# Performance work log

Hardware: AMD Instinct MI355X
Metric: run time of the kernel (lower is better)

Reference implementation:

```python
import jax, jax.numpy as jnp
import numpy as np

B, T, C, H = 4, 2048, 768, 12
HD = C // H  # 64
EPS = 1e-5


def layer_norm(x, g, b):
    mu = jnp.mean(x, axis=-1, keepdims=True)
    var = jnp.var(x, axis=-1, keepdims=True)
    return (x - mu) * jax.lax.rsqrt(var + EPS) * g + b


def setup_inputs() -> dict:
    key = jax.random.key(0)
    ks = jax.random.split(key, 14)
    s_c = 1.0 / np.sqrt(C)
    s_4c = 1.0 / np.sqrt(4 * C)
    return {
        "x": jax.random.normal(ks[0], (B, T, C), jnp.float32),
        # per-head Q/K/V projections stacked over heads [H, C, HD]
        "wq": jax.random.uniform(ks[1], (H, C, HD), jnp.float32, -s_c, s_c),
        "bq": jnp.zeros((H, HD), jnp.float32),
        "wk": jax.random.uniform(ks[2], (H, C, HD), jnp.float32, -s_c, s_c),
        "bk": jnp.zeros((H, HD), jnp.float32),
        "wv": jax.random.uniform(ks[3], (H, C, HD), jnp.float32, -s_c, s_c),
        "bv": jnp.zeros((H, HD), jnp.float32),
        "w_proj": jax.random.uniform(ks[4], (C, C), jnp.float32, -s_c, s_c),
        "b_proj": jnp.zeros((C,), jnp.float32),
        "w1": jax.random.uniform(ks[5], (C, 4 * C), jnp.float32, -s_c, s_c),
        "b1": jnp.zeros((4 * C,), jnp.float32),
        "w2": jax.random.uniform(ks[6], (4 * C, C), jnp.float32, -s_4c, s_4c),
        "b2": jnp.zeros((C,), jnp.float32),
        "g1": jnp.ones((C,), jnp.float32),
        "beta1": jnp.zeros((C,), jnp.float32),
        "g2": jnp.ones((C,), jnp.float32),
        "beta2": jnp.zeros((C,), jnp.float32),
    }


def reference(x, wq, bq, wk, bk, wv, bv, w_proj, b_proj, w1, b1, w2, b2, g1, beta1, g2, beta2):
    # --- attention sublayer ---
    h = layer_norm(x, g1, beta1)
    q = jnp.einsum('btc,hcd->bhtd', h, wq) + bq[None, :, None, :]
    k = jnp.einsum('btc,hcd->bhtd', h, wk) + bk[None, :, None, :]
    v = jnp.einsum('btc,hcd->bhtd', h, wv) + bv[None, :, None, :]
    # NOTE: source applies NO 1/sqrt(head_size) scaling
    scores = jnp.einsum('bhtd,bhsd->bhts', q, k)  # [B,H,T,T]
    causal = jnp.tril(jnp.ones((T, T), bool))
    scores = jnp.where(causal, scores, -jnp.inf)
    wei = jax.nn.softmax(scores, axis=-1)
    attn = jnp.einsum('bhts,bhsd->bhtd', wei, v)  # [B,H,T,HD]
    attn = attn.transpose(0, 2, 1, 3).reshape(B, T, C)  # concat heads
    x = x + attn @ w_proj + b_proj
    # --- MLP sublayer ---
    h2 = layer_norm(x, g2, beta2)
    x = x + jax.nn.relu(h2 @ w1 + b1) @ w2 + b2
    return x
```

## Files before the change

### kernel.cpp

```cpp
#include <hip/hip_runtime.h>
#include <hip/hip_bf16.h>
#include <math.h>

#define BB 4
#define TT 2048
#define CC 768
#define HH 12
#define HDIM 64
#define C4 3072
#define MM (BB*TT)
#define EPSL 1e-5f

typedef __bf16 bf16x8 __attribute__((ext_vector_type(8)));
typedef float f32x4 __attribute__((ext_vector_type(4)));

__device__ __forceinline__ ushort f2bf(float f) {
    union { float f; unsigned u; } v; v.f = f;
    unsigned r = v.u + 0x7fffu + ((v.u >> 16) & 1u);
    return (ushort)(r >> 16);
}

__device__ __forceinline__ void glds16(const void* g, void* l) {
    __builtin_amdgcn_global_load_lds(
        (const __attribute__((address_space(1))) void*)g,
        (__attribute__((address_space(3))) void*)l, 16, 0, 0);
}

#define WVM(N) asm volatile("s_waitcnt vmcnt(" #N ")" ::: "memory")
#define WLG0   asm volatile("s_waitcnt lgkmcnt(0)" ::: "memory")

__device__ __forceinline__ void pbar() {
    __builtin_amdgcn_sched_barrier(0);
    __builtin_amdgcn_s_barrier();
    __builtin_amdgcn_sched_barrier(0);
}

__global__ __launch_bounds__(256) void ln_k(const float* __restrict__ X,
                                            const float* __restrict__ G,
                                            const float* __restrict__ Be,
                                            ushort* __restrict__ O)
{
    int row = blockIdx.x;
    const float* xr = X + (size_t)row * CC;
    int t = threadIdx.x;
    float v0 = xr[t], v1 = xr[t + 256], v2 = xr[t + 512];
    float s  = v0 + v1 + v2;
    float sq = v0*v0 + v1*v1 + v2*v2;
    #pragma unroll
    for (int off = 32; off; off >>= 1) {
        s  += __shfl_xor(s,  off);
        sq += __shfl_xor(sq, off);
    }
    __shared__ float red[8];
    int wv = t >> 6, ln = t & 63;
    if (ln == 0) { red[wv] = s; red[4 + wv] = sq; }
    __syncthreads();
    s  = red[0] + red[1] + red[2] + red[3];
    sq = red[4] + red[5] + red[6] + red[7];
    float mu  = s * (1.0f / CC);
    float var = sq * (1.0f / CC) - mu * mu;
    float rs  = rsqrtf(var + EPSL);
    ushort* orow = O + (size_t)row * CC;
    orow[t]       = f2bf((v0 - mu) * rs * G[t]       + Be[t]);
    orow[t + 256] = f2bf((v1 - mu) * rs * G[t + 256] + Be[t + 256]);
    orow[t + 512] = f2bf((v2 - mu) * rs * G[t + 512] + Be[t + 512]);
}

template<int MODE>
__global__ __launch_bounds__(256) void repack_k(const float* __restrict__ W,
                                                ushort* __restrict__ WT,
                                                int K, int N, int outStride)
{
    __shared__ float tl[64][65];
    int n0 = blockIdx.x * 64, k0 = blockIdx.y * 64;
    int c = threadIdx.x & 63, rr = threadIdx.x >> 6;
    #pragma unroll
    for (int i = 0; i < 16; ++i) {
        int r = i * 4 + rr;
        float v;
        if (MODE == 0) v = W[(size_t)(k0 + r) * N + n0 + c];
        else           v = W[((size_t)(n0 >> 6) * CC + k0 + r) * 64 + c];
        tl[r][c] = v;
    }
    __syncthreads();
    #pragma unroll
    for (int i = 0; i < 16; ++i) {
        int r = i * 4 + rr;
        WT[(size_t)(n0 + r) * outStride + k0 + c] = f2bf(tl[c][r]);
    }
}

template<int EPI>
__global__ __launch_bounds__(512, 2) void gemm8p(
    const ushort* __restrict__ A, const ushort* __restrict__ BT,
    int M, int N, int K,
    void* __restrict__ ov0, void* __restrict__ ov1, void* __restrict__ ov2,
    const float* __restrict__ bias0, const float* __restrict__ bias1,
    const float* __restrict__ bias2,
    const float* __restrict__ resid, ushort* __restrict__ obf)
{
    __shared__ ushort lds[2][2][256 * 64];

    int nbx = gridDim.x;
    int nwg = nbx * gridDim.y;
    int orig = blockIdx.y * nbx + blockIdx.x;
    int cpx = nwg >> 3;
    int swz = (orig & 7) * cpx + (orig >> 3);
    int bn = swz % nbx, bm = swz / nbx;

    int tid = threadIdx.x;
    int lane = tid & 63;
    int w = tid >> 6;
    int wrow = (w >> 2) * 128, wcol = (w & 3) * 64;
    int fr = lane & 15, kh = lane >> 4;
    int rxor = (fr & 7) * 8;

    const size_t aR0 = (size_t)bm * 256;
    const size_t bR0 = (size_t)bn * 256;
    const int nt = K >> 6;

    int srow = tid >> 3;
    int scol = (tid & 7) * 8;
    int gcol = scol ^ ((srow & 7) * 8);

    f32x4 acc[8][4] = {};

    {
        glds16(BT + (bR0 +   0 + srow) * K + gcol, &lds[0][1][(  0 + srow) * 64 + scol]);
        glds16(BT + (bR0 +  64 + srow) * K + gcol, &lds[0][1][( 64 + srow) * 64 + scol]);
        glds16(BT + (bR0 + 128 + srow) * K + gcol, &lds[0][1][(128 + srow) * 64 + scol]);
        glds16(BT + (bR0 + 192 + srow) * K + gcol, &lds[0][1][(192 + srow) * 64 + scol]);
        glds16(A  + (aR0 +   0 + srow) * K + gcol, &lds[0][0][(  0 + srow) * 64 + scol]);
        glds16(A  + (aR0 + 128 + srow) * K + gcol, &lds[0][0][(128 + srow) * 64 + scol]);
        glds16(A  + (aR0 +  64 + srow) * K + gcol, &lds[0][0][( 64 + srow) * 64 + scol]);
        glds16(A  + (aR0 + 192 + srow) * K + gcol, &lds[0][0][(192 + srow) * 64 + scol]);
    }
    WVM(2);
    pbar();

    for (int t = 0; t < nt; ++t) {
        int slot = t & 1, nslot = slot ^ 1;
        int kst = (t + 1) << 6;
        bool st = (t + 1) < nt;
        const ushort* Asl = &lds[slot][0][0];
        const ushort* Bsl = &lds[slot][1][0];
        bf16x8 aF[4][2];
        #pragma unroll
        for (int p = 0; p < 4; ++p) {
            const int rh = p >> 1, ch = p & 1;
            if (ch == 0) {
                #pragma unroll
                for (int i = 0; i < 4; ++i)
                    #pragma unroll
                    for (int k2 = 0; k2 < 2; ++k2) {
                        int R = wrow + rh * 64 + i * 16 + fr;
                        aF[i][k2] = *(const bf16x8*)&Asl[R * 64 + ((k2 * 32 + kh * 8) ^ rxor)];
                    }
            }
            bf16x8 bF[2][2];
            #pragma unroll
            for (int j2 = 0; j2 < 2; ++j2)
                #pragma unroll
                for (int k2 = 0; k2 < 2; ++k2) {
                    int Rb = wcol + ch * 32 + j2 * 16 + fr;
                    bF[j2][k2] = *(const bf16x8*)&Bsl[Rb * 64 + ((k2 * 32 + kh * 8) ^ rxor)];
                }
            if (st) {
                if (p == 0) {
                    glds16(BT + (bR0 +   0 + srow) * K + kst + gcol, &lds[nslot][1][(  0 + srow) * 64 + scol]);
                    glds16(BT + (bR0 +  64 + srow) * K + kst + gcol, &lds[nslot][1][( 64 + srow) * 64 + scol]);
                } else if (p == 1) {
                    glds16(BT + (bR0 + 128 + srow) * K + kst + gcol, &lds[nslot][1][(128 + srow) * 64 + scol]);
                    glds16(BT + (bR0 + 192 + srow) * K + kst + gcol, &lds[nslot][1][(192 + srow) * 64 + scol]);
                } else if (p == 2) {
                    glds16(A  + (aR0 +   0 + srow) * K + kst + gcol, &lds[nslot][0][(  0 + srow) * 64 + scol]);
                    glds16(A  + (aR0 + 128 + srow) * K + kst + gcol, &lds[nslot][0][(128 + srow) * 64 + scol]);
                } else {
                    glds16(A  + (aR0 +  64 + srow) * K + kst + gcol, &lds[nslot][0][( 64 + srow) * 64 + scol]);
                    glds16(A  + (aR0 + 192 + srow) * K + kst + gcol, &lds[nslot][0][(192 + srow) * 64 + scol]);
                }
            }
            __builtin_amdgcn_s_setprio(1);
            #pragma unroll
            for (int i = 0; i < 4; ++i)
                #pragma unroll
                for (int j2 = 0; j2 < 2; ++j2)
                    #pragma unroll
                    for (int k2 = 0; k2 < 2; ++k2)
                        acc[rh * 4 + i][ch * 2 + j2] = __builtin_amdgcn_mfma_f32_16x16x32_bf16(
                            aF[i][k2], bF[j2][k2], acc[rh * 4 + i][ch * 2 + j2], 0, 0, 0);
            __builtin_amdgcn_s_setprio(0);
            if (p == 1) { if (st) { WVM(4); } else { WVM(0); } }
            else if (p == 3) { WVM(2); }
            WLG0;
            pbar();
        }
    }

    if (EPI == 1) {
        int seg = bn / 3;
        ushort* op = (ushort*)(seg == 0 ? ov0 : (seg == 1 ? ov1 : ov2));
        const float* bsp = seg == 0 ? bias0 : (seg == 1 ? bias1 : bias2);
        int cb = (bn - seg * 3) * 256 + wcol;
        int h = cb >> 6;
        #pragma unroll
        for (int ri = 0; ri < 8; ++ri) {
            int row0 = bm * 256 + wrow + ri * 16 + kh * 4;
            int b = row0 >> 11;
            int t0 = row0 & (TT - 1);
            #pragma unroll
            for (int cj = 0; cj < 4; ++cj) {
                int d = cj * 16 + fr;
                float bsv = bsp[h * 64 + d];
                #pragma unroll
                for (int r = 0; r < 4; ++r)
                    op[((size_t)(b * HH + h) * TT + t0 + r) * 64 + d] =
                        f2bf(acc[ri][cj][r] + bsv);
            }
        }
    } else if (EPI == 2) {
        float* o0 = (float*)ov0;
        #pragma unroll
        for (int ri = 0; ri < 8; ++ri) {
            int row0 = bm * 256 + wrow + ri * 16 + kh * 4;
            #pragma unroll
            for (int cj = 0; cj < 4; ++cj) {
                int col = bn * 256 + wcol + cj * 16 + fr;
                float bsv = bias0[col];
                #pragma unroll
                for (int r = 0; r < 4; ++r) {
                    size_t idx = (size_t)(row0 + r) * N + col;
                    o0[idx] = acc[ri][cj][r] + bsv + resid[idx];
                }
            }
        }
    } else {
        #pragma unroll
        for (int ri = 0; ri < 8; ++ri) {
            int row0 = bm * 256 + wrow + ri * 16 + kh * 4;
            #pragma unroll
            for (int cj = 0; cj < 4; ++cj) {
                int col = bn * 256 + wcol + cj * 16 + fr;
                float bsv = bias0[col];
                #pragma unroll
                for (int r = 0; r < 4; ++r) {
                    float v = fmaxf(acc[ri][cj][r] + bsv, 0.f);
                    obf[(size_t)(row0 + r) * N + col] = f2bf(v);
                }
            }
        }
    }
}

__global__ __launch_bounds__(256) void vtrans_k(const ushort* __restrict__ V,
                                                ushort* __restrict__ Vt)
{
    __shared__ ushort tl[64][72];
    int blk = blockIdx.x;
    int tt = blk & 31, bh = blk >> 5;
    size_t base = (size_t)bh * TT * 64;
    int t0 = tt * 64;
    int e = threadIdx.x;
    int rr = e >> 3, cc8 = (e & 7) * 8;
    #pragma unroll
    for (int p = 0; p < 2; ++p) {
        int t = p * 32 + rr;
        *(uint4*)&tl[t][cc8] = *(const uint4*)&V[base + (size_t)(t0 + t) * 64 + cc8];
    }
    __syncthreads();
    #pragma unroll
    for (int p = 0; p < 2; ++p) {
        int d = p * 32 + rr;
        ushort tmp[8];
        #pragma unroll
        for (int i = 0; i < 8; ++i) tmp[i] = tl[cc8 + i][d];
        *(uint4*)&Vt[base + (size_t)d * TT + t0 + cc8] = *(uint4*)tmp;
    }
}

__global__ __launch_bounds__(256) void attn_k(const ushort* __restrict__ Q,
                                              const ushort* __restrict__ Kb,
                                              const ushort* __restrict__ Vt,
                                              ushort* __restrict__ Ob)
{
    __shared__ ushort Kl[64][72];
    __shared__ ushort Vl[64][72];
    __shared__ ushort Pl[4][16][72];

    int orig = blockIdx.x;
    int swz = (orig & 7) * 96 + (orig >> 3);
    int pair = swz & 15;
    int bh = swz >> 4;
    int b = bh / HH, h = bh - b * HH;
    int tid = threadIdx.x, lane = tid & 63, w = tid >> 6;
    int c = lane & 15, g = lane >> 4;
    size_t base = (size_t)bh * TT * 64;
    int srow = tid >> 3, scol = (tid & 7) * 8;
    const float LOG2E = 1.44269504088896340736f;

    #pragma unroll
    for (int sel = 0; sel < 2; ++sel) {
        int qt = sel ? (31 - pair) : pair;
        int q0 = qt * 64;

        bf16x8 aq[2];
        #pragma unroll
        for (int kc = 0; kc < 2; ++kc) {
            bf16x8 raw = *(const bf16x8*)&Q[base + (size_t)(q0 + w * 16 + c) * 64 + kc * 32 + g * 8];
            #pragma unroll
            for (int e = 0; e < 8; ++e)
                raw[e] = (__bf16)((float)raw[e] * LOG2E);
            aq[kc] = raw;
        }

        f32x4 oa[4] = {};
        float mrun[4] = {-INFINITY, -INFINITY, -INFINITY, -INFINITY};
        float lrun[4] = {0.f, 0.f, 0.f, 0.f};

        for (int kv0 = 0; kv0 <= q0; kv0 += 64) {
            __syncthreads();
            #pragma unroll
            for (int p = 0; p < 2; ++p) {
                int r = p * 32 + srow;
                *(uint4*)&Kl[r][scol] = *(const uint4*)&Kb[base + (size_t)(kv0 + r) * 64 + scol];
                *(uint4*)&Vl[r][scol] = *(const uint4*)&Vt[base + (size_t)r * TT + kv0 + scol];
            }
            __syncthreads();

            f32x4 sa[4] = {};
            #pragma unroll
            for (int kc = 0; kc < 2; ++kc)
                #pragma unroll
                for (int j = 0; j < 4; ++j) {
                    bf16x8 kf = *(const bf16x8*)&Kl[j * 16 + c][kc * 32 + g * 8];
                    sa[j] = __builtin_amdgcn_mfma_f32_16x16x32_bf16(aq[kc], kf, sa[j], 0, 0, 0);
                }

            if (kv0 == q0) {
                #pragma unroll
                for (int j = 0; j < 4; ++j)
                    #pragma unroll
                    for (int r = 0; r < 4; ++r)
                        if (j * 16 + c > w * 16 + g * 4 + r) sa[j][r] = -1e30f;
            }

            float vlmax = sa[0][0];
            #pragma unroll
            for (int j = 0; j < 4; ++j)
                #pragma unroll
                for (int r = 0; r < 4; ++r) vlmax = fmaxf(vlmax, sa[j][r]);
            float mmin = fminf(fminf(mrun[0], mrun[1]), fminf(mrun[2], mrun[3]));
            if (!__all(vlmax <= mmin + 11.5f)) {
                #pragma unroll
                for (int r = 0; r < 4; ++r) {
                    float m0 = fmaxf(fmaxf(sa[0][r], sa[1][r]), fmaxf(sa[2][r], sa[3][r]));
                    #pragma unroll
                    for (int off = 8; off; off >>= 1) m0 = fmaxf(m0, __shfl_xor(m0, off));
                    float mnew = fmaxf(mrun[r], m0);
                    float sc = __builtin_amdgcn_exp2f(mrun[r] - mnew);
                    lrun[r] *= sc;
                    #pragma unroll
                    for (int j = 0; j < 4; ++j) oa[j][r] *= sc;
                    mrun[r] = mnew;
                }
            }
            #pragma unroll
            for (int r = 0; r < 4; ++r) {
                float ps = 0.f;
                #pragma unroll
                for (int j = 0; j < 4; ++j) {
                    float p = __builtin_amdgcn_exp2f(sa[j][r] - mrun[r]);
                    sa[j][r] = p;
                    ps += p;
                }
                lrun[r] += ps;
            }

            #pragma unroll
            for (int r = 0; r < 4; ++r)
                #pragma unroll
                for (int j = 0; j < 4; ++j)
                    Pl[w][g * 4 + r][j * 16 + c] = (ushort)__builtin_bit_cast(unsigned short, (__bf16)sa[j][r]);

            bf16x8 pf[2];
            #pragma unroll
            for (int kc = 0; kc < 2; ++kc)
                pf[kc] = *(const bf16x8*)&Pl[w][c][kc * 32 + g * 8];

            #pragma unroll
            for (int kc = 0; kc < 2; ++kc)
                #pragma unroll
                for (int j = 0; j < 4; ++j) {
                    bf16x8 vf = *(const bf16x8*)&Vl[j * 16 + c][kc * 32 + g * 8];
                    oa[j] = __builtin_amdgcn_mfma_f32_16x16x32_bf16(pf[kc], vf, oa[j], 0, 0, 0);
                }
        }

        float inv[4];
        #pragma unroll
        for (int r = 0; r < 4; ++r) {
            float l = lrun[r];
            #pragma unroll
            for (int off = 8; off; off >>= 1) l += __shfl_xor(l, off);
            inv[r] = 1.0f / l;
        }
        size_t orow = (size_t)b * TT + q0 + w * 16;
        #pragma unroll
        for (int j = 0; j < 4; ++j)
            #pragma unroll
            for (int r = 0; r < 4; ++r) {
                float v = oa[j][r] * inv[r];
                Ob[(orow + g * 4 + r) * CC + h * 64 + j * 16 + c] = f2bf(v);
            }
    }
}

extern "C" void kernel_launch(void* const* d_in, const int* in_sizes, int n_in,
                              void* d_out, int out_size, void* d_ws, size_t ws_size,
                              hipStream_t stream)
{
    const float* x   = (const float*)d_in[0];
    const float* wq  = (const float*)d_in[1];
    const float* bq  = (const float*)d_in[2];
    const float* wk  = (const float*)d_in[3];
    const float* bk  = (const float*)d_in[4];
    const float* wvw = (const float*)d_in[5];
    const float* bv  = (const float*)d_in[6];
    const float* wp  = (const float*)d_in[7];
    const float* bp  = (const float*)d_in[8];
    const float* w1  = (const float*)d_in[9];
    const float* b1  = (const float*)d_in[10];
    const float* w2  = (const float*)d_in[11];
    const float* b2  = (const float*)d_in[12];
    const float* g1  = (const float*)d_in[13];
    const float* be1 = (const float*)d_in[14];
    const float* g2  = (const float*)d_in[15];
    const float* be2 = (const float*)d_in[16];

    float* out = (float*)d_out;
    const size_t S = (size_t)MM * CC;

    ushort* wsu   = (ushort*)d_ws;
    ushort* WTqkv = wsu;
    ushort* WTp   = WTqkv + (size_t)2304 * 768;
    ushort* WT1   = WTp   + (size_t)768 * 768;
    ushort* WT2   = WT1   + (size_t)3072 * 768;
    ushort* hbf   = WT2   + (size_t)768 * 3072;
    ushort* attnb = hbf   + S;
    ushort* qb    = attnb + S;
    ushort* kb    = qb + S;
    ushort* vb    = kb + S;
    ushort* vtb   = vb + S;
    ushort* midb  = qb;

    dim3 rg(12, 12);
    repack_k<1><<<rg, 256, 0, stream>>>(wq,  WTqkv,                      768, 768, 768);
    repack_k<1><<<rg, 256, 0, stream>>>(wk,  WTqkv + (size_t)768*768,    768, 768, 768);
    repack_k<1><<<rg, 256, 0, stream>>>(wvw, WTqkv + (size_t)2*768*768,  768, 768, 768);
    repack_k<0><<<rg, 256, 0, stream>>>(wp,  WTp, 768, 768, 768);
    repack_k<0><<<dim3(48, 12), 256, 0, stream>>>(w1, WT1, 768, 3072, 768);
    repack_k<0><<<dim3(12, 48), 256, 0, stream>>>(w2, WT2, 3072, 768, 3072);

    ln_k<<<MM, 256, 0, stream>>>(x, g1, be1, hbf);
    gemm8p<1><<<dim3(9, 32), 512, 0, stream>>>(hbf, WTqkv, MM, 2304, CC,
        qb, kb, vb, bq, bk, bv, nullptr, nullptr);
    vtrans_k<<<48 * 32, 256, 0, stream>>>(vb, vtb);
    attn_k<<<48 * 16, 256, 0, stream>>>(qb, kb, vtb, attnb);
    gemm8p<2><<<dim3(3, 32), 512, 0, stream>>>(attnb, WTp, MM, CC, CC,
        out, nullptr, nullptr, bp, nullptr, nullptr, x, nullptr);

    ln_k<<<MM, 256, 0, stream>>>(out, g2, be2, hbf);
    gemm8p<3><<<dim3(12, 32), 512, 0, stream>>>(hbf, WT1, MM, C4, CC,
        nullptr, nullptr, nullptr, b1, nullptr, nullptr, nullptr, midb);
    gemm8p<2><<<dim3(3, 32), 512, 0, stream>>>(midb, WT2, MM, CC, C4,
        out, nullptr, nullptr, b2, nullptr, nullptr, out, nullptr);
}
```

Measured before the change: 316.9 us.

## Split-K the narrow N=768 GEMMs and fuse partial-sum reduction into LayerNorm

The projection and second MLP GEMMs use only 96 workgroups, so the K dimension is split in two with gridDim.z. The upper slice writes fp32 partials to scratch. For the projection, the partial is folded into a new ln_add_k that adds the residual and computes LayerNorm in one pass. For W2, a separate vector add kernel merges the partial. The prefetch schedule is also regrouped so all B loads issue in phase 0 and all A loads in phase 1, with the wait counts adjusted. The extra fp32 partial traffic and the additional add kernel are the cost.

```diff
diff --git a/kernel.cpp b/kernel.cpp
--- a/kernel.cpp
+++ b/kernel.cpp
@@ -66,6 +66,56 @@
     orow[t + 512] = f2bf((v2 - mu) * rs * G[t + 512] + Be[t + 512]);
 }
 
+__global__ __launch_bounds__(256) void ln_add_k(float* __restrict__ X,
+                                                const float* __restrict__ P,
+                                                const float* __restrict__ G,
+                                                const float* __restrict__ Be,
+                                                ushort* __restrict__ O)
+{
+    int row = blockIdx.x;
+    float* xr = X + (size_t)row * CC;
+    const float* pr = P + (size_t)row * CC;
+    int t = threadIdx.x;
+    float v0 = xr[t]       + pr[t];
+    float v1 = xr[t + 256] + pr[t + 256];
+    float v2 = xr[t + 512] + pr[t + 512];
+    xr[t] = v0; xr[t + 256] = v1; xr[t + 512] = v2;
+    float s  = v0 + v1 + v2;
+    float sq = v0*v0 + v1*v1 + v2*v2;
+    #pragma unroll
+    for (int off = 32; off; off >>= 1) {
+        s  += __shfl_xor(s,  off);
+        sq += __shfl_xor(sq, off);
+    }
+    __shared__ float red[8];
+    int wv = t >> 6, ln = t & 63;
+    if (ln == 0) { red[wv] = s; red[4 + wv] = sq; }
+    __syncthreads();
+    s  = red[0] + red[1] + red[2] + red[3];
+    sq = red[4] + red[5] + red[6] + red[7];
+    float mu  = s * (1.0f / CC);
+    float var = sq * (1.0f / CC) - mu * mu;
+    float rs  = rsqrtf(var + EPSL);
+    ushort* orow = O + (size_t)row * CC;
+    orow[t]       = f2bf((v0 - mu) * rs * G[t]       + Be[t]);
+    orow[t + 256] = f2bf((v1 - mu) * rs * G[t + 256] + Be[t + 256]);
+    orow[t + 512] = f2bf((v2 - mu) * rs * G[t + 512] + Be[t + 512]);
+}
+
+__global__ __launch_bounds__(256) void addto_k(float* __restrict__ o,
+                                               const float* __restrict__ p,
+                                               int n4)
+{
+    int i = blockIdx.x * 256 + threadIdx.x;
+    int stride = gridDim.x * 256;
+    for (; i < n4; i += stride) {
+        float4 a = ((const float4*)o)[i];
+        float4 b = ((const float4*)p)[i];
+        a.x += b.x; a.y += b.y; a.z += b.z; a.w += b.w;
+        ((float4*)o)[i] = a;
+    }
+}
+
 template<int MODE>
 __global__ __launch_bounds__(256) void repack_k(const float* __restrict__ W,
                                                 ushort* __restrict__ WT,
@@ -97,16 +147,19 @@
     void* __restrict__ ov0, void* __restrict__ ov1, void* __restrict__ ov2,
     const float* __restrict__ bias0, const float* __restrict__ bias1,
     const float* __restrict__ bias2,
-    const float* __restrict__ resid, ushort* __restrict__ obf)
+    const float* __restrict__ resid, ushort* __restrict__ obf,
+    float* __restrict__ part)
 {
     __shared__ ushort lds[2][2][256 * 64];
 
     int nbx = gridDim.x;
-    int nwg = nbx * gridDim.y;
-    int orig = blockIdx.y * nbx + blockIdx.x;
+    int nwg = nbx * gridDim.y * gridDim.z;
+    int orig = (blockIdx.z * gridDim.y + blockIdx.y) * nbx + blockIdx.x;
     int cpx = nwg >> 3;
     int swz = (orig & 7) * cpx + (orig >> 3);
-    int bn = swz % nbx, bm = swz / nbx;
+    int zi = swz / (nbx * gridDim.y);
+    int rem = swz - zi * nbx * gridDim.y;
+    int bn = rem % nbx, bm = rem / nbx;
 
     int tid = threadIdx.x;
     int lane = tid & 63;
@@ -117,11 +170,13 @@
 
     const size_t aR0 = (size_t)bm * 256;
     const size_t bR0 = (size_t)bn * 256;
-    const int nt = K >> 6;
+    const int Ksl = K / (int)gridDim.z;
+    const int koff = zi * Ksl;
+    const int nt = Ksl >> 6;
 
     int srow = tid >> 3;
     int scol = (tid & 7) * 8;
-    int gcol = scol ^ ((srow & 7) * 8);
+    int gcol = koff + (scol ^ ((srow & 7) * 8));
 
     f32x4 acc[8][4] = {};
 
@@ -140,7 +195,7 @@
 
     for (int t = 0; t < nt; ++t) {
         int slot = t & 1, nslot = slot ^ 1;
-        int kst = (t + 1) << 6;
+        int kst = gcol + ((t + 1) << 6);
         bool st = (t + 1) < nt;
         const ushort* Asl = &lds[slot][0][0];
         const ushort* Bsl = &lds[slot][1][0];
@@ -167,17 +222,15 @@
                 }
             if (st) {
                 if (p == 0) {
-                    glds16(BT + (bR0 +   0 + srow) * K + kst + gcol, &lds[nslot][1][(  0 + srow) * 64 + scol]);
-                    glds16(BT + (bR0 +  64 + srow) * K + kst + gcol, &lds[nslot][1][( 64 + srow) * 64 + scol]);
+                    glds16(BT + (bR0 +   0 + srow) * K + kst, &lds[nslot][1][(  0 + srow) * 64 + scol]);
+                    glds16(BT + (bR0 +  64 + srow) * K + kst, &lds[nslot][1][( 64 + srow) * 64 + scol]);
+                    glds16(BT + (bR0 + 128 + srow) * K + kst, &lds[nslot][1][(128 + srow) * 64 + scol]);
+                    glds16(BT + (bR0 + 192 + srow) * K + kst, &lds[nslot][1][(192 + srow) * 64 + scol]);
                 } else if (p == 1) {
-                    glds16(BT + (bR0 + 128 + srow) * K + kst + gcol, &lds[nslot][1][(128 + srow) * 64 + scol]);
-                    glds16(BT + (bR0 + 192 + srow) * K + kst + gcol, &lds[nslot][1][(192 + srow) * 64 + scol]);
-                } else if (p == 2) {
-                    glds16(A  + (aR0 +   0 + srow) * K + kst + gcol, &lds[nslot][0][(  0 + srow) * 64 + scol]);
-                    glds16(A  + (aR0 + 128 + srow) * K + kst + gcol, &lds[nslot][0][(128 + srow) * 64 + scol]);
-                } else {
-                    glds16(A  + (aR0 +  64 + srow) * K + kst + gcol, &lds[nslot][0][( 64 + srow) * 64 + scol]);
-                    glds16(A  + (aR0 + 192 + srow) * K + kst + gcol, &lds[nslot][0][(192 + srow) * 64 + scol]);
+                    glds16(A  + (aR0 +   0 + srow) * K + kst, &lds[nslot][0][(  0 + srow) * 64 + scol]);
+                    glds16(A  + (aR0 + 128 + srow) * K + kst, &lds[nslot][0][(128 + srow) * 64 + scol]);
+                    glds16(A  + (aR0 +  64 + srow) * K + kst, &lds[nslot][0][( 64 + srow) * 64 + scol]);
+                    glds16(A  + (aR0 + 192 + srow) * K + kst, &lds[nslot][0][(192 + srow) * 64 + scol]);
                 }
             }
             __builtin_amdgcn_s_setprio(1);
@@ -190,14 +243,26 @@
                         acc[rh * 4 + i][ch * 2 + j2] = __builtin_amdgcn_mfma_f32_16x16x32_bf16(
                             aF[i][k2], bF[j2][k2], acc[rh * 4 + i][ch * 2 + j2], 0, 0, 0);
             __builtin_amdgcn_s_setprio(0);
-            if (p == 1) { if (st) { WVM(4); } else { WVM(0); } }
-            else if (p == 3) { WVM(2); }
+            if (p == 1) { if (st) { WVM(8); } else { WVM(0); } }
+            else if (p == 3) { if (st) { WVM(2); } }
             WLG0;
             pbar();
         }
     }
 
-    if (EPI == 1) {
+    if (gridDim.z > 1 && zi > 0) {
+        #pragma unroll
+        for (int ri = 0; ri < 8; ++ri) {
+            int row0 = bm * 256 + wrow + ri * 16 + kh * 4;
+            #pragma unroll
+            for (int cj = 0; cj < 4; ++cj) {
+                int col = bn * 256 + wcol + cj * 16 + fr;
+                #pragma unroll
+                for (int r = 0; r < 4; ++r)
+                    part[(size_t)(row0 + r) * N + col] = acc[ri][cj][r];
+            }
+        }
+    } else if (EPI == 1) {
         int seg = bn / 3;
         ushort* op = (ushort*)(seg == 0 ? ov0 : (seg == 1 ? ov1 : ov2));
         const float* bsp = seg == 0 ? bias0 : (seg == 1 ? bias1 : bias2);
@@ -452,6 +517,8 @@
     ushort* vb    = kb + S;
     ushort* vtb   = vb + S;
     ushort* midb  = qb;
+    float*  part_proj = (float*)qb;
+    float*  part_w2   = (float*)hbf;
 
     dim3 rg(12, 12);
     repack_k<1><<<rg, 256, 0, stream>>>(wq,  WTqkv,                      768, 768, 768);
@@ -462,16 +529,17 @@
     repack_k<0><<<dim3(12, 48), 256, 0, stream>>>(w2, WT2, 3072, 768, 3072);
 
     ln_k<<<MM, 256, 0, stream>>>(x, g1, be1, hbf);
-    gemm8p<1><<<dim3(9, 32), 512, 0, stream>>>(hbf, WTqkv, MM, 2304, CC,
-        qb, kb, vb, bq, bk, bv, nullptr, nullptr);
+    gemm8p<1><<<dim3(9, 32, 1), 512, 0, stream>>>(hbf, WTqkv, MM, 2304, CC,
+        qb, kb, vb, bq, bk, bv, nullptr, nullptr, nullptr);
     vtrans_k<<<48 * 32, 256, 0, stream>>>(vb, vtb);
     attn_k<<<48 * 16, 256, 0, stream>>>(qb, kb, vtb, attnb);
-    gemm8p<2><<<dim3(3, 32), 512, 0, stream>>>(attnb, WTp, MM, CC, CC,
-        out, nullptr, nullptr, bp, nullptr, nullptr, x, nullptr);
-
-    ln_k<<<MM, 256, 0, stream>>>(out, g2, be2, hbf);
-    gemm8p<3><<<dim3(12, 32), 512, 0, stream>>>(hbf, WT1, MM, C4, CC,
-        nullptr, nullptr, nullptr, b1, nullptr, nullptr, nullptr, midb);
-    gemm8p<2><<<dim3(3, 32), 512, 0, stream>>>(midb, WT2, MM, CC, C4,
-        out, nullptr, nullptr, b2, nullptr, nullptr, out, nullptr);
-}
+    gemm8p<2><<<dim3(3, 32, 2), 512, 0, stream>>>(attnb, WTp, MM, CC, CC,
+        out, nullptr, nullptr, bp, nullptr, nullptr, x, nullptr, part_proj);
+
+    ln_add_k<<<MM, 256, 0, stream>>>(out, part_proj, g2, be2, hbf);
+    gemm8p<3><<<dim3(12, 32, 1), 512, 0, stream>>>(hbf, WT1, MM, C4, CC,
+        nullptr, nullptr, nullptr, b1, nullptr, nullptr, nullptr, midb, nullptr);
+    gemm8p<2><<<dim3(3, 32, 2), 512, 0, stream>>>(midb, WT2, MM, CC, C4,
+        out, nullptr, nullptr, b2, nullptr, nullptr, out, nullptr, part_w2);
+    addto_k<<<2048, 256, 0, stream>>>(out, part_w2, MM * CC / 4);
+}
```

Result: faster. 303.7 us (-4.2%).
